# Performance work log

Hardware: AMD Instinct MI355X
Metric: run time of the kernel (lower is better)

Reference implementation:

```python
import jax, jax.numpy as jnp
import numpy as np

B = 16384
S = 7
CELL = 1.0 / 7.0   # CELL_SILE
LC = 5.0           # lambda_coord
LN = 0.5           # lambda_noobj


def setup_inputs() -> dict:
    key = jax.random.key(0)
    k1, k2, k3 = jax.random.split(key, 3)
    predictions = jax.random.normal(k1, (B, S, S, 30), dtype=jnp.float32)
    targets = jax.random.uniform(k2, (B, S, S, 30), dtype=jnp.float32)
    # channel 4 is the objectness flag; code requires it to be exactly 0 or 1
    conf = (jax.random.uniform(k3, (B, S, S)) < 0.25).astype(jnp.float32)
    targets = targets.at[..., 4].set(conf)
    return {"predictions": predictions, "targets": targets}


def _box_corners(xy, wh):
    # Faithful to the original in-place bug: x2y2 uses the ALREADY-UPDATED x1y1
    xy1 = xy * CELL - wh * 0.5
    xy2 = xy1 * CELL + wh * 0.5
    return xy1, xy2


def _loss_terms(predictions, targets):
    p = predictions.reshape(-1, 30)   # [N, 30], N = B*S*S
    t = targets.reshape(-1, 30)
    obj = (t[:, 4] == 1.0).astype(p.dtype)
    noobj = (t[:, 4] == 0.0).astype(p.dtype)

    # no-object confidence loss on cols 4 and 9
    noobj_loss = LN * jnp.sum(noobj * (jnp.square(p[:, 4] - t[:, 4]) + jnp.square(p[:, 9] - t[:, 9])))

    # two predicted boxes per cell: cols 0:4 and 5:9 ; wh are sqrt-encoded -> square
    pb = jnp.stack([p[:, 0:4], p[:, 5:9]], axis=1)        # [N, 2, 4]
    pxy1, pxy2 = _box_corners(pb[..., 0:2], jnp.square(pb[..., 2:4]))  # [N,2,2]
    txy1, txy2 = _box_corners(t[:, None, 0:2], jnp.square(t[:, None, 2:4]))  # [N,1,2]

    # torchvision.ops.box_iou math (no clamp on areas, clamp(0) on intersection)
    lt = jnp.maximum(pxy1, txy1)
    rb = jnp.minimum(pxy2, txy2)
    inter = jnp.prod(jnp.clip(rb - lt, 0.0, None), axis=-1)   # [N, 2]
    area_p = jnp.prod(pxy2 - pxy1, axis=-1)                   # [N, 2]
    area_t = jnp.prod(txy2 - txy1, axis=-1)                   # [N, 1]
    iou = inter / (area_p + area_t - inter)                   # [N, 2]

    idx = jnp.argmax(iou, axis=1)                             # responsible box in {0,1}

    cols = idx[:, None] * 5 + jnp.arange(4)[None, :]          # [N, 4]
    cp = jnp.take_along_axis(p, cols, axis=1)
    ct = jnp.take_along_axis(t, cols, axis=1)
    center_loss = LC * jnp.sum(obj * jnp.sum(jnp.square(cp[:, 0:2] - ct[:, 0:2]), axis=1))
    wh_loss = LC * jnp.sum(obj * jnp.sum(jnp.square(cp[:, 2:4] - ct[:, 2:4]), axis=1))

    ccol = (idx * 5 + 4)[:, None]
    conf_loss = LC * jnp.sum(obj * jnp.square(jnp.take_along_axis(p, ccol, axis=1) - jnp.take_along_axis(t, ccol, axis=1))[:, 0])

    kcol = (jnp.argmax(t[:, 10:30], axis=1) + 10)[:, None]
    cls_loss = LC * jnp.sum(obj * jnp.square(jnp.take_along_axis(p, kcol, axis=1) - jnp.take_along_axis(t, kcol, axis=1))[:, 0])

    total = noobj_loss + center_loss + wh_loss + conf_loss + cls_loss
    return cls_loss, conf_loss, center_loss + wh_loss, total


def reference(predictions, targets):
    return _loss_terms(predictions, targets)
```

## Files before the change

kernel.cpp:

```cpp
#include <hip/hip_runtime.h>


constexpr int   BLK  = 256;
constexpr int   NC   = 16384 * 7 * 7;
constexpr int   GRID = NC / BLK;
constexpr float CELL = 1.0f / 7.0f;
constexpr float LC   = 5.0f;
constexpr float LN   = 0.5f;

__launch_bounds__(BLK, 8)
__global__ void yolo_partial(const float* __restrict__ P, const float* __restrict__ T,
                             float4* __restrict__ ws)
{
    const int tid  = threadIdx.x;
    const int cell = blockIdx.x * BLK + tid;
    const float* trow = T + (size_t)cell * 30;
    const float* prow = P + (size_t)cell * 30;

    float tv[30];
    #pragma unroll
    for (int j = 0; j < 15; ++j) {
        float2 v = reinterpret_cast<const float2*>(trow)[j];
        tv[2 * j] = v.x; tv[2 * j + 1] = v.y;
    }
    float pv[10];
    #pragma unroll
    for (int j = 0; j < 5; ++j) {
        float2 v = reinterpret_cast<const float2*>(prow)[j];
        pv[2 * j] = v.x; pv[2 * j + 1] = v.y;
    }

    int kc = 10;
    float best = tv[10];
    #pragma unroll
    for (int k = 11; k < 30; ++k) {
        if (tv[k] > best) { best = tv[k]; kc = k; }
    }
    float2 pg = *reinterpret_cast<const float2*>(prow + (kc & ~1));
    float pk = (kc & 1) ? pg.y : pg.x;

    const float t4 = tv[4];
    const float obj   = (t4 == 1.0f) ? 1.0f : 0.0f;
    const float noobj = (t4 == 0.0f) ? 1.0f : 0.0f;

    float d4 = pv[4] - t4;
    float d9 = pv[9] - tv[9];
    float a_noobj = noobj * (d4 * d4 + d9 * d9);

    float tw2 = tv[2] * tv[2], th2 = tv[3] * tv[3];
    float tx1 = tv[0] * CELL - 0.5f * tw2;
    float tx2 = tx1 * CELL + 0.5f * tw2;
    float ty1 = tv[1] * CELL - 0.5f * th2;
    float ty2 = ty1 * CELL + 0.5f * th2;
    float area_t = (tx2 - tx1) * (ty2 - ty1);

    float iou0, iou1;
    #pragma unroll
    for (int b = 0; b < 2; ++b) {
        float bw2 = pv[5 * b + 2] * pv[5 * b + 2];
        float bh2 = pv[5 * b + 3] * pv[5 * b + 3];
        float px1 = pv[5 * b + 0] * CELL - 0.5f * bw2;
        float px2 = px1 * CELL + 0.5f * bw2;
        float py1 = pv[5 * b + 1] * CELL - 0.5f * bh2;
        float py2 = py1 * CELL + 0.5f * bh2;
        float ltx = fmaxf(px1, tx1), lty = fmaxf(py1, ty1);
        float rbx = fminf(px2, tx2), rby = fminf(py2, ty2);
        float inter = fmaxf(rbx - ltx, 0.0f) * fmaxf(rby - lty, 0.0f);
        float area_p = (px2 - px1) * (py2 - py1);
        float iou = inter / (area_p + area_t - inter);
        if (b == 0) iou0 = iou; else iou1 = iou;
    }
    const bool b1 = (iou1 > iou0);

    float cpx = b1 ? pv[5] : pv[0], ctx = b1 ? tv[5] : tv[0];
    float cpy = b1 ? pv[6] : pv[1], cty = b1 ? tv[6] : tv[1];
    float cpw = b1 ? pv[7] : pv[2], ctw = b1 ? tv[7] : tv[2];
    float cph = b1 ? pv[8] : pv[3], cth = b1 ? tv[8] : tv[3];
    float cpc = b1 ? pv[9] : pv[4], ctc = b1 ? tv[9] : tv[4];

    float dx = cpx - ctx, dy = cpy - cty;
    float dw = cpw - ctw, dh = cph - cth;
    float a_cw   = obj * (dx * dx + dy * dy + dw * dw + dh * dh);
    float dc = cpc - ctc;
    float a_conf = obj * dc * dc;
    float dk = pk - best;
    float a_cls  = obj * dk * dk;

    float vals[4] = { a_cls, a_conf, a_cw, a_noobj };
    #pragma unroll
    for (int c = 0; c < 4; ++c) {
        #pragma unroll
        for (int off = 32; off > 0; off >>= 1)
            vals[c] += __shfl_down(vals[c], off, 64);
    }
    __shared__ float red[4][4];
    const int wave = tid >> 6;
    if ((tid & 63) == 0) {
        red[0][wave] = vals[0]; red[1][wave] = vals[1];
        red[2][wave] = vals[2]; red[3][wave] = vals[3];
    }
    __syncthreads();
    if (tid == 0) {
        ws[blockIdx.x] = make_float4(
            red[0][0] + red[0][1] + red[0][2] + red[0][3],
            red[1][0] + red[1][1] + red[1][2] + red[1][3],
            red[2][0] + red[2][1] + red[2][2] + red[2][3],
            red[3][0] + red[3][1] + red[3][2] + red[3][3]);
    }
}

__launch_bounds__(1024, 1)
__global__ void yolo_reduce(const float4* __restrict__ ws, float* __restrict__ out)
{
    __shared__ float red[4][16];
    const int tid = threadIdx.x;

    float s0 = 0.f, s1 = 0.f, s2 = 0.f, s3 = 0.f;
    for (int b = tid; b < GRID; b += 1024) {
        float4 v = ws[b];
        s0 += v.x; s1 += v.y; s2 += v.z; s3 += v.w;
    }
    float vals[4] = { s0, s1, s2, s3 };
    #pragma unroll
    for (int c = 0; c < 4; ++c) {
        #pragma unroll
        for (int off = 32; off > 0; off >>= 1)
            vals[c] += __shfl_down(vals[c], off, 64);
        if ((tid & 63) == 0) red[c][tid >> 6] = vals[c];
    }
    __syncthreads();
    if (tid == 0) {
        float t0 = 0.f, t1 = 0.f, t2 = 0.f, t3 = 0.f;
        #pragma unroll
        for (int w = 0; w < 16; ++w) {
            t0 += red[0][w]; t1 += red[1][w]; t2 += red[2][w]; t3 += red[3][w];
        }
        out[0] = LC * t0;
        out[1] = LC * t1;
        out[2] = LC * t2;
        out[3] = LN * t3 + LC * (t0 + t1 + t2);
    }
}

extern "C" void kernel_launch(void* const* d_in, const int* in_sizes, int n_in,
                              void* d_out, int out_size, void* d_ws, size_t ws_size,
                              hipStream_t stream) {
    const float* P = (const float*)d_in[0];
    const float* T = (const float*)d_in[1];
    float* out = (float*)d_out;
    float4* ws = (float4*)d_ws;

    yolo_partial<<<GRID, BLK, 0, stream>>>(P, T, ws);
    yolo_reduce<<<1, 1024, 0, stream>>>(ws, out);
}
```

Before: 207.2 us.

## Stage tiles through LDS with direct global-to-LDS loads in persistent blocks

Replaces per-thread strided row loads with coalesced 16-byte global_load_lds copies of 128-cell tiles of targets and predictions into shared memory. Each thread then reads its 30-float rows from LDS, and a grid-stride persistent loop accumulates partial sums across tiles. The aim is fully coalesced DRAM access instead of scattered 120-byte-stride float2 loads. In exchange it now loads all 30 prediction channels rather than about 12, adds two barriers per tile, and has strided LDS reads that can cause bank conflicts.

```diff
diff --git a/kernel.cpp b/kernel.cpp
--- a/kernel.cpp
+++ b/kernel.cpp
@@ -1,90 +1,113 @@
 #include <hip/hip_runtime.h>
 
 
-constexpr int   BLK  = 256;
-constexpr int   NC   = 16384 * 7 * 7;
-constexpr int   GRID = NC / BLK;
-constexpr float CELL = 1.0f / 7.0f;
-constexpr float LC   = 5.0f;
-constexpr float LN   = 0.5f;
+constexpr int   BLK   = 128;
+constexpr int   TILE  = 128;
+constexpr int   NC    = 16384 * 7 * 7;
+constexpr int   NTILE = NC / TILE;
+constexpr int   GRID  = 3136;
+constexpr float CELL  = 1.0f / 7.0f;
+constexpr float LC    = 5.0f;
+constexpr float LN    = 0.5f;
 
-__launch_bounds__(BLK, 8)
+__device__ inline void gload_lds16(const float4* g, float4* l)
+{
+    __builtin_amdgcn_global_load_lds(
+        (const __attribute__((address_space(1))) void*)g,
+        (__attribute__((address_space(3))) void*)l,
+        16, 0, 0);
+}
+
+__launch_bounds__(BLK, 3)
 __global__ void yolo_partial(const float* __restrict__ P, const float* __restrict__ T,
                              float4* __restrict__ ws)
 {
-    const int tid  = threadIdx.x;
-    const int cell = blockIdx.x * BLK + tid;
-    const float* trow = T + (size_t)cell * 30;
-    const float* prow = P + (size_t)cell * 30;
+    __shared__ float4 s4[1920];
+    __shared__ float red[4][2];
 
-    float tv[30];
-    #pragma unroll
-    for (int j = 0; j < 15; ++j) {
-        float2 v = reinterpret_cast<const float2*>(trow)[j];
-        tv[2 * j] = v.x; tv[2 * j + 1] = v.y;
+    const int tid = threadIdx.x;
+    float a_cls = 0.f, a_conf = 0.f, a_cw = 0.f, a_noobj = 0.f;
+
+    for (int t = blockIdx.x; t < NTILE; t += GRID) {
+        const size_t fbase = (size_t)t * (TILE * 30);
+        const float4* gT = reinterpret_cast<const float4*>(T + fbase);
+        const float4* gP = reinterpret_cast<const float4*>(P + fbase);
+
+        #pragma unroll
+        for (int k = 0; k < 15; ++k) {
+            const int idx = k * BLK + tid;
+            const float4* g = (idx < 960) ? (gT + idx) : (gP + (idx - 960));
+            gload_lds16(g, s4 + idx);
+        }
+        __syncthreads();
+
+        const float* sf  = reinterpret_cast<const float*>(s4);
+        const float* myT = sf + (size_t)tid * 30;
+        const float* myP = sf + 3840 + (size_t)tid * 30;
+        float tv[30], pv[30];
+        #pragma unroll
+        for (int j = 0; j < 15; ++j) {
+            float2 a = reinterpret_cast<const float2*>(myT)[j];
+            tv[2 * j] = a.x; tv[2 * j + 1] = a.y;
+            float2 b = reinterpret_cast<const float2*>(myP)[j];
+            pv[2 * j] = b.x; pv[2 * j + 1] = b.y;
+        }
+
+        float best = tv[10], pk = pv[10];
+        #pragma unroll
+        for (int k = 11; k < 30; ++k) {
+            if (tv[k] > best) { best = tv[k]; pk = pv[k]; }
+        }
+
+        const float t4    = tv[4];
+        const float obj   = (t4 == 1.0f) ? 1.0f : 0.0f;
+        const float noobj = (t4 == 0.0f) ? 1.0f : 0.0f;
+
+        float d4 = pv[4] - t4;
+        float d9 = pv[9] - tv[9];
+        a_noobj += noobj * (d4 * d4 + d9 * d9);
+
+        float tw2 = tv[2] * tv[2], th2 = tv[3] * tv[3];
+        float tx1 = tv[0] * CELL - 0.5f * tw2;
+        float tx2 = tx1 * CELL + 0.5f * tw2;
+        float ty1 = tv[1] * CELL - 0.5f * th2;
+        float ty2 = ty1 * CELL + 0.5f * th2;
+        float area_t = (tx2 - tx1) * (ty2 - ty1);
+
+        float iou0, iou1;
+        #pragma unroll
+        for (int b = 0; b < 2; ++b) {
+            float bw2 = pv[5 * b + 2] * pv[5 * b + 2];
+            float bh2 = pv[5 * b + 3] * pv[5 * b + 3];
+            float px1 = pv[5 * b + 0] * CELL - 0.5f * bw2;
+            float px2 = px1 * CELL + 0.5f * bw2;
+            float py1 = pv[5 * b + 1] * CELL - 0.5f * bh2;
+            float py2 = py1 * CELL + 0.5f * bh2;
+            float ltx = fmaxf(px1, tx1), lty = fmaxf(py1, ty1);
+            float rbx = fminf(px2, tx2), rby = fminf(py2, ty2);
+            float inter = fmaxf(rbx - ltx, 0.0f) * fmaxf(rby - lty, 0.0f);
+            float area_p = (px2 - px1) * (py2 - py1);
+            float iou = inter / (area_p + area_t - inter);
+            if (b == 0) iou0 = iou; else iou1 = iou;
+        }
+        const bool b1 = (iou1 > iou0);
+
+        float cpx = b1 ? pv[5] : pv[0], ctx = b1 ? tv[5] : tv[0];
+        float cpy = b1 ? pv[6] : pv[1], cty = b1 ? tv[6] : tv[1];
+        float cpw = b1 ? pv[7] : pv[2], ctw = b1 ? tv[7] : tv[2];
+        float cph = b1 ? pv[8] : pv[3], cth = b1 ? tv[8] : tv[3];
+        float cpc = b1 ? pv[9] : pv[4], ctc = b1 ? tv[9] : tv[4];
+
+        float dx = cpx - ctx, dy = cpy - cty;
+        float dw = cpw - ctw, dh = cph - cth;
+        a_cw   += obj * (dx * dx + dy * dy + dw * dw + dh * dh);
+        float dc = cpc - ctc;
+        a_conf += obj * dc * dc;
+        float dk = pk - best;
+        a_cls  += obj * dk * dk;
+
+        __syncthreads();
     }
-    float pv[10];
-    #pragma unroll
-    for (int j = 0; j < 5; ++j) {
-        float2 v = reinterpret_cast<const float2*>(prow)[j];
-        pv[2 * j] = v.x; pv[2 * j + 1] = v.y;
-    }
-
-    int kc = 10;
-    float best = tv[10];
-    #pragma unroll
-    for (int k = 11; k < 30; ++k) {
-        if (tv[k] > best) { best = tv[k]; kc = k; }
-    }
-    float2 pg = *reinterpret_cast<const float2*>(prow + (kc & ~1));
-    float pk = (kc & 1) ? pg.y : pg.x;
-
-    const float t4 = tv[4];
-    const float obj   = (t4 == 1.0f) ? 1.0f : 0.0f;
-    const float noobj = (t4 == 0.0f) ? 1.0f : 0.0f;
-
-    float d4 = pv[4] - t4;
-    float d9 = pv[9] - tv[9];
-    float a_noobj = noobj * (d4 * d4 + d9 * d9);
-
-    float tw2 = tv[2] * tv[2], th2 = tv[3] * tv[3];
-    float tx1 = tv[0] * CELL - 0.5f * tw2;
-    float tx2 = tx1 * CELL + 0.5f * tw2;
-    float ty1 = tv[1] * CELL - 0.5f * th2;
-    float ty2 = ty1 * CELL + 0.5f * th2;
-    float area_t = (tx2 - tx1) * (ty2 - ty1);
-
-    float iou0, iou1;
-    #pragma unroll
-    for (int b = 0; b < 2; ++b) {
-        float bw2 = pv[5 * b + 2] * pv[5 * b + 2];
-        float bh2 = pv[5 * b + 3] * pv[5 * b + 3];
-        float px1 = pv[5 * b + 0] * CELL - 0.5f * bw2;
-        float px2 = px1 * CELL + 0.5f * bw2;
-        float py1 = pv[5 * b + 1] * CELL - 0.5f * bh2;
-        float py2 = py1 * CELL + 0.5f * bh2;
-        float ltx = fmaxf(px1, tx1), lty = fmaxf(py1, ty1);
-        float rbx = fminf(px2, tx2), rby = fminf(py2, ty2);
-        float inter = fmaxf(rbx - ltx, 0.0f) * fmaxf(rby - lty, 0.0f);
-        float area_p = (px2 - px1) * (py2 - py1);
-        float iou = inter / (area_p + area_t - inter);
-        if (b == 0) iou0 = iou; else iou1 = iou;
-    }
-    const bool b1 = (iou1 > iou0);
-
-    float cpx = b1 ? pv[5] : pv[0], ctx = b1 ? tv[5] : tv[0];
-    float cpy = b1 ? pv[6] : pv[1], cty = b1 ? tv[6] : tv[1];
-    float cpw = b1 ? pv[7] : pv[2], ctw = b1 ? tv[7] : tv[2];
-    float cph = b1 ? pv[8] : pv[3], cth = b1 ? tv[8] : tv[3];
-    float cpc = b1 ? pv[9] : pv[4], ctc = b1 ? tv[9] : tv[4];
-
-    float dx = cpx - ctx, dy = cpy - cty;
-    float dw = cpw - ctw, dh = cph - cth;
-    float a_cw   = obj * (dx * dx + dy * dy + dw * dw + dh * dh);
-    float dc = cpc - ctc;
-    float a_conf = obj * dc * dc;
-    float dk = pk - best;
-    float a_cls  = obj * dk * dk;
 
     float vals[4] = { a_cls, a_conf, a_cw, a_noobj };
     #pragma unroll
@@ -93,7 +116,6 @@
         for (int off = 32; off > 0; off >>= 1)
             vals[c] += __shfl_down(vals[c], off, 64);
     }
-    __shared__ float red[4][4];
     const int wave = tid >> 6;
     if ((tid & 63) == 0) {
         red[0][wave] = vals[0]; red[1][wave] = vals[1];
@@ -101,11 +123,10 @@
     }
     __syncthreads();
     if (tid == 0) {
-        ws[blockIdx.x] = make_float4(
-            red[0][0] + red[0][1] + red[0][2] + red[0][3],
-            red[1][0] + red[1][1] + red[1][2] + red[1][3],
-            red[2][0] + red[2][1] + red[2][2] + red[2][3],
-            red[3][0] + red[3][1] + red[3][2] + red[3][3]);
+        ws[blockIdx.x] = make_float4(red[0][0] + red[0][1],
+                                     red[1][0] + red[1][1],
+                                     red[2][0] + red[2][1],
+                                     red[3][0] + red[3][1]);
     }
 }
 
```

Measured after the change: 205.5 us. Within noise of the previous version (-0.8%).
